# Optimization experiments

Hardware: AMD Instinct MI355X
Metric: run time of the kernel (lower is better)

Reference implementation:

```python
import jax, jax.numpy as jnp
import numpy as np

B, N, C = 4, 4000, 91          # images, proposals/image, classes (incl. background)
H = W = 800                    # image shape
WX, WY, WW, WH = 10.0, 10.0, 5.0, 5.0   # bbox_reg_weights
BBOX_CLIP = float(np.log(1000.0 / 16.0))
SCORE_T = 0.05
NMS_T = 0.5
DETS = 100                     # detections_per_img
MIN_SIZE = 0.01
NEG = jnp.float32(-1e30)
M = N * (C - 1)                # candidates per image after dropping background


def setup_inputs() -> dict:
    key = jax.random.key(0)
    k1, k2, k3, k4 = jax.random.split(key, 4)
    class_logits = jax.random.normal(k1, (B * N, C), jnp.float32)
    box_regression = jax.random.normal(k2, (B * N, C * 4), jnp.float32)
    # valid proposals: x1<x2, y1<y2, inside the image
    ctr = jax.random.uniform(k3, (B, N, 2), jnp.float32, 0.0, 800.0)
    wh = jax.random.uniform(k4, (B, N, 2), jnp.float32, 16.0, 256.0)
    x1y1 = jnp.clip(ctr - 0.5 * wh, 0.0, 800.0)
    x2y2 = jnp.clip(ctr + 0.5 * wh, 0.0, 800.0)
    proposals = jnp.concatenate([x1y1, x2y2], axis=-1)
    return {"class_logits": class_logits, "box_regression": box_regression,
            "proposals": proposals}


def _decode(rel, props):
    # rel: [B,N,C,4] deltas, props: [B,N,4] -> per-class boxes [B,N,C,4]
    widths = props[..., 2] - props[..., 0]
    heights = props[..., 3] - props[..., 1]
    ctr_x = props[..., 0] + 0.5 * widths
    ctr_y = props[..., 1] + 0.5 * heights
    dx = rel[..., 0] / WX
    dy = rel[..., 1] / WY
    dw = jnp.minimum(rel[..., 2] / WW, BBOX_CLIP)
    dh = jnp.minimum(rel[..., 3] / WH, BBOX_CLIP)
    pcx = dx * widths[..., None] + ctr_x[..., None]
    pcy = dy * heights[..., None] + ctr_y[..., None]
    pw = jnp.exp(dw) * widths[..., None]
    ph = jnp.exp(dh) * heights[..., None]
    return jnp.stack([pcx - 0.5 * pw, pcy - 0.5 * ph,
                      pcx + 0.5 * pw, pcy + 0.5 * ph], axis=-1)


def _iou_one(box, boxes):
    # box [4] vs boxes [M,4]
    lt = jnp.maximum(box[:2], boxes[:, :2])
    rb = jnp.minimum(box[2:], boxes[:, 2:])
    wh = jnp.clip(rb - lt, 0.0)
    inter = wh[:, 0] * wh[:, 1]
    a1 = (box[2] - box[0]) * (box[3] - box[1])
    a2 = (boxes[:, 2] - boxes[:, 0]) * (boxes[:, 3] - boxes[:, 1])
    return inter / (a1 + a2 - inter)


def _nms_image(boxes_off, scores_m):
    # greedy NMS on class-offset boxes; returns DETS indices + validity flags
    idxs = jnp.arange(scores_m.shape[0])

    def step(scores_rem, _):
        best = jnp.argmax(scores_rem)
        bscore = scores_rem[best]
        iou = _iou_one(boxes_off[best], boxes_off)
        sup = (iou > NMS_T) | (idxs == best)
        return jnp.where(sup, NEG, scores_rem), (best, bscore > NEG * 0.5)

    _, (keep_idx, keep_ok) = jax.lax.scan(step, scores_m, None, length=DETS)
    return keep_idx, keep_ok


def reference(class_logits, box_regression, proposals):
    logits = class_logits.reshape(B, N, C)
    rel = box_regression.reshape(B, N, C, 4)
    boxes = _decode(rel, proposals)                       # [B,N,C,4]
    # clip_boxes_to_image
    boxes = jnp.stack([jnp.clip(boxes[..., 0], 0.0, W),
                       jnp.clip(boxes[..., 1], 0.0, H),
                       jnp.clip(boxes[..., 2], 0.0, W),
                       jnp.clip(boxes[..., 3], 0.0, H)], axis=-1)
    scores = jax.nn.softmax(logits, axis=-1)              # [B,N,C]
    # drop background class 0, flatten per-image candidates
    cand_boxes = boxes[:, :, 1:, :].reshape(B, M, 4)
    cand_scores = scores[:, :, 1:].reshape(B, M)
    labels = jnp.tile(jnp.arange(1, C, dtype=jnp.int32), N)   # [M]
    # score threshold + remove_small_boxes
    ws = cand_boxes[..., 2] - cand_boxes[..., 0]
    hs = cand_boxes[..., 3] - cand_boxes[..., 1]
    valid = (cand_scores > SCORE_T) & (ws >= MIN_SIZE) & (hs >= MIN_SIZE)
    scores_m = jnp.where(valid, cand_scores, NEG)
    # batched_nms: offset boxes per class so cross-class boxes never overlap
    offs = labels.astype(jnp.float32) * (W + 1.0)
    boxes_off = cand_boxes + offs[None, :, None]
    keep_idx, keep_ok = jax.vmap(_nms_image)(boxes_off, scores_m)  # [B,DETS]
    out_boxes = jnp.take_along_axis(cand_boxes, keep_idx[..., None], axis=1)
    out_scores = jnp.take_along_axis(cand_scores, keep_idx, axis=1)
    out_labels = labels[keep_idx]
    out_boxes = jnp.where(keep_ok[..., None], out_boxes, 0.0)
    out_scores = jnp.where(keep_ok, out_scores, 0.0)
    out_labels = jnp.where(keep_ok, out_labels, 0)
    return out_boxes, out_scores, out_labels, keep_ok
```

## Files before the change

### kernel.cpp

```cpp
#include <hip/hip_runtime.h>

#define Bc 4
#define Nc 4000
#define Cc 91
#define SEGW 20
#define BCAP 64
#define SELTGT 512
#define DETS 100
#define NBIN 4096
#define SELCAP 1024

typedef unsigned long long u64;

__device__ __forceinline__ float4 decode_box(const float4 r, float w, float h,
                                             float cx, float cy) {
    const float BBOX_CLIP = 4.135166556742356f;
    float dx = r.x / 10.f, dy = r.y / 10.f;
    float dw = fminf(r.z / 5.f, BBOX_CLIP);
    float dh = fminf(r.w / 5.f, BBOX_CLIP);
    float pcx = dx * w + cx, pcy = dy * h + cy;
    float pw = expf(dw) * w, ph = expf(dh) * h;
    float4 o;
    o.x = fminf(fmaxf(pcx - 0.5f * pw, 0.f), 800.f);
    o.y = fminf(fmaxf(pcy - 0.5f * ph, 0.f), 800.f);
    o.z = fminf(fmaxf(pcx + 0.5f * pw, 0.f), 800.f);
    o.w = fminf(fmaxf(pcy + 0.5f * ph, 0.f), 800.f);
    return o;
}

__global__ __launch_bounds__(256) void compact_k(
    const float* __restrict__ logits, const float* __restrict__ regs,
    const float* __restrict__ props, ulonglong2* __restrict__ pmask,
    unsigned* __restrict__ scoreseg, int* __restrict__ ghist,
    int* __restrict__ bcnt) {
    if (blockIdx.x < 16) {
        int base = blockIdx.x * 1024;
#pragma unroll
        for (int j = 0; j < 4; ++j)
            ghist[base + j * 256 + threadIdx.x] = 0;
    } else if (blockIdx.x == 16) {
        int t = threadIdx.x;
        bcnt[t] = 0;
        if (t < Bc * Cc - 256) bcnt[256 + t] = 0;
    }
    const int wv = threadIdx.x >> 6;
    const int ln = threadIdx.x & 63;
    const int pA = blockIdx.x * 8 + wv * 2;
    const int pB = pA + 1;

    const float* lA = logits + (size_t)pA * Cc;
    const float* lB = logits + (size_t)pB * Cc;
    float a0 = lA[ln];
    float b0 = lB[ln];
    float a1 = (ln < Cc - 64) ? lA[64 + ln] : -1e30f;
    float b1 = (ln < Cc - 64) ? lB[64 + ln] : -1e30f;
    const float4 prA = *reinterpret_cast<const float4*>(props + 4 * (size_t)pA);
    const float4 prB = *reinterpret_cast<const float4*>(props + 4 * (size_t)pB);

    float mA = fmaxf(a0, a1), mB = fmaxf(b0, b1);
#pragma unroll
    for (int off = 32; off; off >>= 1) {
        mA = fmaxf(mA, __shfl_xor(mA, off));
        mB = fmaxf(mB, __shfl_xor(mB, off));
    }
    float eA0 = expf(a0 - mA), eB0 = expf(b0 - mB);
    float eA1 = (ln < Cc - 64) ? expf(a1 - mA) : 0.f;
    float eB1 = (ln < Cc - 64) ? expf(b1 - mB) : 0.f;
    float sA = eA0 + eA1, sB = eB0 + eB1;
#pragma unroll
    for (int off = 32; off; off >>= 1) {
        sA += __shfl_xor(sA, off);
        sB += __shfl_xor(sB, off);
    }

    const float wA = prA.z - prA.x, hA = prA.w - prA.y;
    const float cxA = prA.x + 0.5f * wA, cyA = prA.y + 0.5f * hA;
    const float wB = prB.z - prB.x, hB = prB.w - prB.y;
    const float cxB = prB.x + 0.5f * wB, cyB = prB.y + 0.5f * hB;

    float vA0 = eA0 / sA, vB0 = eB0 / sB, vA1 = eA1 / sA, vB1 = eB1 / sB;
    bool fA0 = false, fA1 = false, fB0 = false, fB1 = false;
    if (ln >= 1 && vA0 > 0.05f) {
        float4 r = *reinterpret_cast<const float4*>(
            regs + ((size_t)pA * Cc + ln) * 4);
        float4 bx = decode_box(r, wA, hA, cxA, cyA);
        fA0 = (bx.z - bx.x >= 0.01f) && (bx.w - bx.y >= 0.01f);
    }
    if (ln >= 1 && vB0 > 0.05f) {
        float4 r = *reinterpret_cast<const float4*>(
            regs + ((size_t)pB * Cc + ln) * 4);
        float4 bx = decode_box(r, wB, hB, cxB, cyB);
        fB0 = (bx.z - bx.x >= 0.01f) && (bx.w - bx.y >= 0.01f);
    }
    if (ln < Cc - 64 && vA1 > 0.05f) {
        float4 r = *reinterpret_cast<const float4*>(
            regs + ((size_t)pA * Cc + 64 + ln) * 4);
        float4 bx = decode_box(r, wA, hA, cxA, cyA);
        fA1 = (bx.z - bx.x >= 0.01f) && (bx.w - bx.y >= 0.01f);
    }
    if (ln < Cc - 64 && vB1 > 0.05f) {
        float4 r = *reinterpret_cast<const float4*>(
            regs + ((size_t)pB * Cc + 64 + ln) * 4);
        float4 bx = decode_box(r, wB, hB, cxB, cyB);
        fB1 = (bx.z - bx.x >= 0.01f) && (bx.w - bx.y >= 0.01f);
    }

    const u64 below = (1ULL << ln) - 1ULL;
    u64 mA0 = __ballot(fA0), mA1 = __ballot(fA1);
    u64 mB0 = __ballot(fB0), mB1 = __ballot(fB1);
    int cA0 = __popcll(mA0), cB0 = __popcll(mB0);
    if (fA0) scoreseg[(size_t)pA * SEGW + __popcll(mA0 & below)] =
        __float_as_uint(vA0);
    if (fA1) scoreseg[(size_t)pA * SEGW + cA0 + __popcll(mA1 & below)] =
        __float_as_uint(vA1);
    if (fB0) scoreseg[(size_t)pB * SEGW + __popcll(mB0 & below)] =
        __float_as_uint(vB0);
    if (fB1) scoreseg[(size_t)pB * SEGW + cB0 + __popcll(mB1 & below)] =
        __float_as_uint(vB1);
    if (ln == 0) {
        pmask[pA] = make_ulonglong2(mA0, mA1);
        pmask[pB] = make_ulonglong2(mB0, mB1);
    }
}

__global__ __launch_bounds__(256) void hist_k(
    const ulonglong2* __restrict__ pmask, const unsigned* __restrict__ scoreseg,
    int* __restrict__ ghist) {
    __shared__ int hist[NBIN];
    const int b = blockIdx.x >> 4;
    const int sub = blockIdx.x & 15;
    const int t = threadIdx.x;
    for (int i = t; i < NBIN; i += 256) hist[i] = 0;
    __syncthreads();
    if (t < 250) {
        int p = b * Nc + sub * 250 + t;
        ulonglong2 pm = pmask[p];
        int nk = __popcll(pm.x) + __popcll(pm.y);
        for (int j = 0; j < nk; ++j)
            atomicAdd(&hist[scoreseg[(size_t)p * SEGW + j] >> 20], 1);
    }
    __syncthreads();
    for (int i = t; i < NBIN; i += 256) {
        int v = hist[i];
        if (v) atomicAdd(&ghist[b * NBIN + i], v);
    }
}

__global__ __launch_bounds__(256) void selthr_k(
    const ulonglong2* __restrict__ pmask, const unsigned* __restrict__ scoreseg,
    const int* __restrict__ ghist, u64* __restrict__ bucket,
    int* __restrict__ bcnt) {
    __shared__ int thrS;
    const int b = blockIdx.x >> 4;
    const int sub = blockIdx.x & 15;
    const int t = threadIdx.x;

    if (t < 64) {
        const int ln = t;
        const int* h = ghist + b * NBIN;
        int loc[64];
        int tot = 0;
#pragma unroll
        for (int j = 0; j < 64; ++j) { loc[j] = h[ln * 64 + j]; tot += loc[j]; }
        int inc = tot;
#pragma unroll
        for (int off = 1; off < 64; off <<= 1) {
            int v = __shfl_down(inc, off);
            if (ln + off < 64) inc += v;
        }
        int cum = inc - tot;
        int myThr = -1;
#pragma unroll
        for (int j = 63; j >= 0; --j) {
            if (cum < SELTGT && cum + loc[j] >= SELTGT) myThr = ln * 64 + j;
            cum += loc[j];
        }
#pragma unroll
        for (int off = 32; off; off >>= 1)
            myThr = max(myThr, __shfl_xor(myThr, off));
        if (ln == 0) thrS = (myThr < 0) ? 0 : myThr;
    }
    __syncthreads();
    const int th = thrS;

    if (t < 250) {
        int p = b * Nc + sub * 250 + t;
        const ulonglong2 pm = pmask[p];
        if (pm.x | pm.y) {
            const int n = p - b * Nc;
            int idx = 0;
#pragma unroll
            for (int rnd = 0; rnd < 2; ++rnd) {
                u64 mm = rnd ? pm.y : pm.x;
                while (mm) {
                    int j = __ffsll((long long)mm) - 1; mm &= mm - 1;
                    int c = j + rnd * 64;
                    unsigned sb = scoreseg[(size_t)p * SEGW + idx]; ++idx;
                    if ((int)(sb >> 20) >= th) {
                        unsigned m = (unsigned)(n * 90 + (c - 1));
                        u64 key = ((u64)sb << 32) |
                                  ((u64)(1048575u - m) << 12) | (u64)c;
                        int sl = atomicAdd(&bcnt[b * Cc + c], 1);
                        if (sl < BCAP) bucket[(b * Cc + c) * BCAP + sl] = key;
                    }
                }
            }
        }
    }
}

__global__ __launch_bounds__(64) void nmsc_k(
    u64* __restrict__ bucket, const int* __restrict__ bcnt,
    const float* __restrict__ regs, const float* __restrict__ props,
    int* __restrict__ kkc) {
    const int b = blockIdx.x / (Cc - 1);
    const int c = 1 + blockIdx.x % (Cc - 1);
    const int ln = threadIdx.x;
    const u64 lkRaw = bucket[(b * Cc + c) * BCAP + ln];
    const int nc = min(bcnt[b * Cc + c], BCAP);
    bool alive = ln < nc;
    u64 lk = alive ? lkRaw : 0ULL;
    int m = 1048575 - (int)((lkRaw >> 12) & 0xFFFFFULL);
    int n = min(max(m / (Cc - 1), 0), Nc - 1);
    int p = b * Nc + n;
    const float4 pr = *reinterpret_cast<const float4*>(props + 4 * (size_t)p);
    float w = pr.z - pr.x, h = pr.w - pr.y;
    float cx = pr.x + 0.5f * w, cy = pr.y + 0.5f * h;
    const float4 r = *reinterpret_cast<const float4*>(
        regs + ((size_t)p * Cc + c) * 4);
    float4 bx = decode_box(r, w, h, cx, cy);
    float off_ = (float)c * 801.0f;
    bx.x += off_; bx.y += off_; bx.z += off_; bx.w += off_;
    float area = (bx.z - bx.x) * (bx.w - bx.y);

    int nk = 0;
    for (;;) {
        u64 mx = alive ? lk : 0ULL;
#pragma unroll
        for (int off = 32; off; off >>= 1) {
            u64 o = __shfl_xor(mx, off);
            mx = (o > mx) ? o : mx;
        }
        if (mx == 0ULL) break;
        u64 wmask = __ballot(alive && lk == mx);
        int wl = __ffsll((long long)wmask) - 1;
        if (ln == wl) bucket[(b * Cc + c) * BCAP + nk] = mx;
        ++nk;
        float wx1 = __shfl(bx.x, wl), wy1 = __shfl(bx.y, wl);
        float wx2 = __shfl(bx.z, wl), wy2 = __shfl(bx.w, wl);
        float wa = __shfl(area, wl);
        if (alive) {
            if (lk == mx) {
                alive = false;
            } else {
                float iw = fmaxf(fminf(wx2, bx.z) - fmaxf(wx1, bx.x), 0.f);
                float ih = fmaxf(fminf(wy2, bx.w) - fmaxf(wy1, bx.y), 0.f);
                float inter = iw * ih;
                float iou = inter / (wa + area - inter);
                if (iou > 0.5f) alive = false;
            }
        }
    }
    if (ln == 0) kkc[b * Cc + c] = nk;
}

__global__ __launch_bounds__(1024) void top100_k(
    const u64* __restrict__ bucket, const int* __restrict__ kkc,
    const float* __restrict__ regs, const float* __restrict__ props,
    float* __restrict__ out) {
    __shared__ u64 sKey[SELCAP];
    __shared__ u64 sTop[DETS];
    __shared__ int cnts[Cc], offs[Cc + 1];
    const int b = blockIdx.x, t = threadIdx.x;
    const int ln = t & 63, wv = t >> 6;

    if (t < Cc)
        cnts[t] = (t == 0) ? 0 : min(max(kkc[b * Cc + t], 0), BCAP);
    if (t < DETS) sTop[t] = 0ULL;
    __syncthreads();
    if (t == 0) {
        int acc = 0;
        for (int c = 0; c < Cc; ++c) { offs[c] = acc; acc += cnts[c]; }
        offs[Cc] = acc;
    }
    __syncthreads();
    const int total = min(offs[Cc], SELCAP);

    for (int c = wv; c < Cc; c += 16) {
        int k = cnts[c];
        if (ln < k) {
            int d = offs[c] + ln;
            if (d >= 0 && d < SELCAP)
                sKey[d] = bucket[(b * Cc + c) * BCAP + ln];
        }
    }
    __syncthreads();

    for (int i = t; i < total; i += 1024) {
        u64 k = sKey[i];
        int r = 0;
#pragma unroll 4
        for (int j = 0; j < total; ++j) r += (sKey[j] > k) ? 1 : 0;
        if (r < DETS) sTop[r] = k;
    }
    __syncthreads();

    if (t < DETS) {
        int o = b * DETS + t;
        u64 k = sTop[t];
        float* ob = out + (size_t)o * 4;
        if (k != 0ULL) {
            int lab = (int)(k & 0xFFFULL);
            int m = 1048575 - (int)((k >> 12) & 0xFFFFFULL);
            int n = m / (Cc - 1);
            int c = m - n * (Cc - 1) + 1;
            int p = b * Nc + n;
            const float4 pr =
                *reinterpret_cast<const float4*>(props + 4 * (size_t)p);
            const float w = pr.z - pr.x, h = pr.w - pr.y;
            const float cx = pr.x + 0.5f * w, cy = pr.y + 0.5f * h;
            const float4 r4 = *reinterpret_cast<const float4*>(
                regs + ((size_t)p * Cc + c) * 4);
            float4 bx = decode_box(r4, w, h, cx, cy);
            ob[0] = bx.x; ob[1] = bx.y; ob[2] = bx.z; ob[3] = bx.w;
            out[Bc * DETS * 4 + o] = __uint_as_float((unsigned)(k >> 32));
            out[Bc * DETS * 5 + o] = (float)lab;
            out[Bc * DETS * 6 + o] = 1.0f;
        } else {
            ob[0] = ob[1] = ob[2] = ob[3] = 0.f;
            out[Bc * DETS * 4 + o] = 0.f;
            out[Bc * DETS * 5 + o] = 0.f;
            out[Bc * DETS * 6 + o] = 0.f;
        }
    }
}

extern "C" void kernel_launch(void* const* d_in, const int* in_sizes, int n_in,
                              void* d_out, int out_size, void* d_ws, size_t ws_size,
                              hipStream_t stream) {
    const float* logits = (const float*)d_in[0];
    const float* regs   = (const float*)d_in[1];
    const float* props  = (const float*)d_in[2];
    float* out = (float*)d_out;

    char* ws = (char*)d_ws;
    size_t o = 0;
    ulonglong2* pmask = (ulonglong2*)(ws + o); o += (size_t)Bc * Nc * 16;
    unsigned* scoreseg = (unsigned*)(ws + o);  o += (size_t)Bc * Nc * SEGW * 4;
    u64* bucket  = (u64*)(ws + o);             o += (size_t)Bc * Cc * BCAP * 8;
    int* ghist   = (int*)(ws + o);             o += (size_t)Bc * NBIN * 4;
    int* bcnt    = (int*)(ws + o);             o += (size_t)Bc * Cc * 4;
    int* kkc     = (int*)(ws + o);

    hipLaunchKernelGGL(compact_k, dim3(Bc * Nc / 8), dim3(256), 0, stream,
                       logits, regs, props, pmask, scoreseg, ghist, bcnt);
    hipLaunchKernelGGL(hist_k, dim3(Bc * 16), dim3(256), 0, stream,
                       pmask, scoreseg, ghist);
    hipLaunchKernelGGL(selthr_k, dim3(Bc * 16), dim3(256), 0, stream,
                       pmask, scoreseg, ghist, bucket, bcnt);
    hipLaunchKernelGGL(nmsc_k, dim3(Bc * (Cc - 1)), dim3(64), 0, stream,
                       bucket, bcnt, regs, props, kkc);
    hipLaunchKernelGGL(top100_k, dim3(Bc), dim3(1024), 0, stream,
                       bucket, kkc, regs, props, out);
}
```

Measured before the change: 52.65 us.

## Fuse histogram into threshold kernel and carry decoded boxes from NMS to top-k

Removes the separate histogram kernel and the global histogram. Each selection block now builds the full per-image score histogram in shared memory with 1024 threads, which also drops the global zeroing and the global atomics. The cost is that the 16 blocks of each image redundantly scan all of that image's proposals. NMS also writes each kept un-offset decoded box into a buffer that aliases the no-longer-needed score segment. The top-100 kernel then reads that box instead of re-reading proposals and regressions and decoding again.

```diff
diff --git a/kernel.cpp b/kernel.cpp
--- a/kernel.cpp
+++ b/kernel.cpp
@@ -31,14 +31,8 @@
 __global__ __launch_bounds__(256) void compact_k(
     const float* __restrict__ logits, const float* __restrict__ regs,
     const float* __restrict__ props, ulonglong2* __restrict__ pmask,
-    unsigned* __restrict__ scoreseg, int* __restrict__ ghist,
-    int* __restrict__ bcnt) {
-    if (blockIdx.x < 16) {
-        int base = blockIdx.x * 1024;
-#pragma unroll
-        for (int j = 0; j < 4; ++j)
-            ghist[base + j * 256 + threadIdx.x] = 0;
-    } else if (blockIdx.x == 16) {
+    unsigned* __restrict__ scoreseg, int* __restrict__ bcnt) {
+    if (blockIdx.x == 16) {
         int t = threadIdx.x;
         bcnt[t] = 0;
         if (t < Bc * Cc - 256) bcnt[256 + t] = 0;
@@ -123,45 +117,33 @@
     }
 }
 
-__global__ __launch_bounds__(256) void hist_k(
+__global__ __launch_bounds__(1024) void selthr_k(
     const ulonglong2* __restrict__ pmask, const unsigned* __restrict__ scoreseg,
-    int* __restrict__ ghist) {
+    u64* __restrict__ bucket, int* __restrict__ bcnt) {
     __shared__ int hist[NBIN];
+    __shared__ int thrS;
     const int b = blockIdx.x >> 4;
     const int sub = blockIdx.x & 15;
     const int t = threadIdx.x;
-    for (int i = t; i < NBIN; i += 256) hist[i] = 0;
-    __syncthreads();
-    if (t < 250) {
-        int p = b * Nc + sub * 250 + t;
+
+    for (int i = t; i < NBIN; i += 1024) hist[i] = 0;
+    __syncthreads();
+
+    for (int pi = t; pi < Nc; pi += 1024) {
+        int p = b * Nc + pi;
         ulonglong2 pm = pmask[p];
         int nk = __popcll(pm.x) + __popcll(pm.y);
         for (int j = 0; j < nk; ++j)
             atomicAdd(&hist[scoreseg[(size_t)p * SEGW + j] >> 20], 1);
     }
     __syncthreads();
-    for (int i = t; i < NBIN; i += 256) {
-        int v = hist[i];
-        if (v) atomicAdd(&ghist[b * NBIN + i], v);
-    }
-}
-
-__global__ __launch_bounds__(256) void selthr_k(
-    const ulonglong2* __restrict__ pmask, const unsigned* __restrict__ scoreseg,
-    const int* __restrict__ ghist, u64* __restrict__ bucket,
-    int* __restrict__ bcnt) {
-    __shared__ int thrS;
-    const int b = blockIdx.x >> 4;
-    const int sub = blockIdx.x & 15;
-    const int t = threadIdx.x;
 
     if (t < 64) {
         const int ln = t;
-        const int* h = ghist + b * NBIN;
         int loc[64];
         int tot = 0;
 #pragma unroll
-        for (int j = 0; j < 64; ++j) { loc[j] = h[ln * 64 + j]; tot += loc[j]; }
+        for (int j = 0; j < 64; ++j) { loc[j] = hist[ln * 64 + j]; tot += loc[j]; }
         int inc = tot;
 #pragma unroll
         for (int off = 1; off < 64; off <<= 1) {
@@ -212,7 +194,7 @@
 __global__ __launch_bounds__(64) void nmsc_k(
     u64* __restrict__ bucket, const int* __restrict__ bcnt,
     const float* __restrict__ regs, const float* __restrict__ props,
-    int* __restrict__ kkc) {
+    float4* __restrict__ kbox, int* __restrict__ kkc) {
     const int b = blockIdx.x / (Cc - 1);
     const int c = 1 + blockIdx.x % (Cc - 1);
     const int ln = threadIdx.x;
@@ -228,9 +210,9 @@
     float cx = pr.x + 0.5f * w, cy = pr.y + 0.5f * h;
     const float4 r = *reinterpret_cast<const float4*>(
         regs + ((size_t)p * Cc + c) * 4);
-    float4 bx = decode_box(r, w, h, cx, cy);
+    const float4 ub = decode_box(r, w, h, cx, cy);
     float off_ = (float)c * 801.0f;
-    bx.x += off_; bx.y += off_; bx.z += off_; bx.w += off_;
+    float4 bx = make_float4(ub.x + off_, ub.y + off_, ub.z + off_, ub.w + off_);
     float area = (bx.z - bx.x) * (bx.w - bx.y);
 
     int nk = 0;
@@ -244,7 +226,10 @@
         if (mx == 0ULL) break;
         u64 wmask = __ballot(alive && lk == mx);
         int wl = __ffsll((long long)wmask) - 1;
-        if (ln == wl) bucket[(b * Cc + c) * BCAP + nk] = mx;
+        if (ln == wl) {
+            bucket[(b * Cc + c) * BCAP + nk] = mx;
+            kbox[(b * Cc + c) * BCAP + nk] = ub;
+        }
         ++nk;
         float wx1 = __shfl(bx.x, wl), wy1 = __shfl(bx.y, wl);
         float wx2 = __shfl(bx.z, wl), wy2 = __shfl(bx.w, wl);
@@ -265,11 +250,12 @@
 }
 
 __global__ __launch_bounds__(1024) void top100_k(
-    const u64* __restrict__ bucket, const int* __restrict__ kkc,
-    const float* __restrict__ regs, const float* __restrict__ props,
-    float* __restrict__ out) {
+    const u64* __restrict__ bucket, const float4* __restrict__ kbox,
+    const int* __restrict__ kkc, float* __restrict__ out) {
     __shared__ u64 sKey[SELCAP];
+    __shared__ float4 sBox[SELCAP];
     __shared__ u64 sTop[DETS];
+    __shared__ int sTopI[DETS];
     __shared__ int cnts[Cc], offs[Cc + 1];
     const int b = blockIdx.x, t = threadIdx.x;
     const int ln = t & 63, wv = t >> 6;
@@ -290,8 +276,10 @@
         int k = cnts[c];
         if (ln < k) {
             int d = offs[c] + ln;
-            if (d >= 0 && d < SELCAP)
+            if (d >= 0 && d < SELCAP) {
                 sKey[d] = bucket[(b * Cc + c) * BCAP + ln];
+                sBox[d] = kbox[(b * Cc + c) * BCAP + ln];
+            }
         }
     }
     __syncthreads();
@@ -301,7 +289,7 @@
         int r = 0;
 #pragma unroll 4
         for (int j = 0; j < total; ++j) r += (sKey[j] > k) ? 1 : 0;
-        if (r < DETS) sTop[r] = k;
+        if (r < DETS) { sTop[r] = k; sTopI[r] = i; }
     }
     __syncthreads();
 
@@ -310,21 +298,10 @@
         u64 k = sTop[t];
         float* ob = out + (size_t)o * 4;
         if (k != 0ULL) {
-            int lab = (int)(k & 0xFFFULL);
-            int m = 1048575 - (int)((k >> 12) & 0xFFFFFULL);
-            int n = m / (Cc - 1);
-            int c = m - n * (Cc - 1) + 1;
-            int p = b * Nc + n;
-            const float4 pr =
-                *reinterpret_cast<const float4*>(props + 4 * (size_t)p);
-            const float w = pr.z - pr.x, h = pr.w - pr.y;
-            const float cx = pr.x + 0.5f * w, cy = pr.y + 0.5f * h;
-            const float4 r4 = *reinterpret_cast<const float4*>(
-                regs + ((size_t)p * Cc + c) * 4);
-            float4 bx = decode_box(r4, w, h, cx, cy);
+            float4 bx = sBox[sTopI[t]];
             ob[0] = bx.x; ob[1] = bx.y; ob[2] = bx.z; ob[3] = bx.w;
             out[Bc * DETS * 4 + o] = __uint_as_float((unsigned)(k >> 32));
-            out[Bc * DETS * 5 + o] = (float)lab;
+            out[Bc * DETS * 5 + o] = (float)(unsigned)(k & 0xFFFULL);
             out[Bc * DETS * 6 + o] = 1.0f;
         } else {
             ob[0] = ob[1] = ob[2] = ob[3] = 0.f;
@@ -346,20 +323,18 @@
     char* ws = (char*)d_ws;
     size_t o = 0;
     ulonglong2* pmask = (ulonglong2*)(ws + o); o += (size_t)Bc * Nc * 16;
-    unsigned* scoreseg = (unsigned*)(ws + o);  o += (size_t)Bc * Nc * SEGW * 4;
+    unsigned* scoreseg = (unsigned*)(ws + o);
+    float4* kbox = (float4*)scoreseg;          o += (size_t)Bc * Nc * SEGW * 4;
     u64* bucket  = (u64*)(ws + o);             o += (size_t)Bc * Cc * BCAP * 8;
-    int* ghist   = (int*)(ws + o);             o += (size_t)Bc * NBIN * 4;
     int* bcnt    = (int*)(ws + o);             o += (size_t)Bc * Cc * 4;
     int* kkc     = (int*)(ws + o);
 
     hipLaunchKernelGGL(compact_k, dim3(Bc * Nc / 8), dim3(256), 0, stream,
-                       logits, regs, props, pmask, scoreseg, ghist, bcnt);
-    hipLaunchKernelGGL(hist_k, dim3(Bc * 16), dim3(256), 0, stream,
-                       pmask, scoreseg, ghist);
-    hipLaunchKernelGGL(selthr_k, dim3(Bc * 16), dim3(256), 0, stream,
-                       pmask, scoreseg, ghist, bucket, bcnt);
+                       logits, regs, props, pmask, scoreseg, bcnt);
+    hipLaunchKernelGGL(selthr_k, dim3(Bc * 16), dim3(1024), 0, stream,
+                       pmask, scoreseg, bucket, bcnt);
     hipLaunchKernelGGL(nmsc_k, dim3(Bc * (Cc - 1)), dim3(64), 0, stream,
-                       bucket, bcnt, regs, props, kkc);
+                       bucket, bcnt, regs, props, kbox, kkc);
     hipLaunchKernelGGL(top100_k, dim3(Bc), dim3(1024), 0, stream,
-                       bucket, kkc, regs, props, out);
-}
+                       bucket, kbox, kkc, out);
+}
```

After: 54.45 us. 1.03x slower.
